# Optimization experiments

Measured on AMD Instinct MI355X. Metric: run time of the kernel, lower is better.

## Reference

```python
import jax, jax.numpy as jnp
import numpy as np
import math

BS, D = 32, 2048  # batch, in_features == out_features (required by the original matmul shapes)
P = 0.5           # DropConnect keep-threshold: mask = (rand <= p)


def setup_inputs() -> dict:
    key = jax.random.key(0)
    kx, kw, kb, kuw, kub = jax.random.split(key, 5)
    stdv = 1.0 / math.sqrt(D)
    x = jax.random.normal(kx, (BS, D), dtype=jnp.float32)
    weight = jax.random.uniform(kw, (D, D), minval=-stdv, maxval=stdv, dtype=jnp.float32)  # (out, in)
    bias = jax.random.uniform(kb, (D,), minval=-stdv, maxval=stdv, dtype=jnp.float32)
    u_w = jax.random.uniform(kuw, (BS, D, D), dtype=jnp.float32)  # per-sample uniforms for weight mask
    u_b = jax.random.uniform(kub, (BS, D), dtype=jnp.float32)     # per-sample uniforms for bias mask
    return {"x": x, "weight": weight, "bias": bias, "u_w": u_w, "u_b": u_b}


def reference(x, weight, bias, u_w, u_b):
    # Training path of DropConnect:
    #   masked_weight[b] = (u_w[b] <= p) * weight            (bs, out, in)
    #   masked_bias[b]   = (u_b[b] <= p) * bias              (bs, out)
    #   y[b] = x[b] @ masked_weight[b] + masked_bias[b]
    # torch.matmul((bs,1,in),(bs,out,in)) contracts x over the 'out' row axis,
    # i.e. y = einsum('bk,bkn->bn') with masked_weight axes (k=out, n=in), valid since out==in.
    wm = (u_w <= P).astype(x.dtype)  # (bs, D, D)
    bm = (u_b <= P).astype(x.dtype)  # (bs, D)
    y = jnp.einsum('bk,bkn->bn', x, wm * weight[None, :, :]) + bm * bias[None, :]
    return y
```

## Files before the change

kernel.cpp:

```cpp
#include <hip/hip_runtime.h>

constexpr int BS = 32;
constexpr int D  = 2048;
constexpr float P = 0.5f;

constexpr int TPB = 256;
constexpr int NPT = 4;
constexpr int NB  = D / (TPB*NPT);
constexpr int KC  = 32;
constexpr int KCH = D / KC;

__global__ __launch_bounds__(TPB) void dropconnect_kernel(
    const float* __restrict__ x,
    const float* __restrict__ weight,
    const float* __restrict__ bias,
    const float* __restrict__ u_w,
    const float* __restrict__ u_b,
    float* __restrict__ out)
{
    const int kc  = blockIdx.x;
    const int nb  = blockIdx.y;
    const int b   = blockIdx.z;
    const int tid = threadIdx.x;

    const int n0 = nb * (TPB * NPT) + tid * NPT;
    const int k0 = kc * KCH;

    __shared__ float xs[KCH];
    if (tid < KCH) xs[tid] = x[b * D + k0 + tid];
    __syncthreads();

    const float4* uw4 = reinterpret_cast<const float4*>(u_w);
    const float4* w4  = reinterpret_cast<const float4*>(weight);
    const int DV = D / 4;

    float acc0 = 0.f, acc1 = 0.f, acc2 = 0.f, acc3 = 0.f;

    size_t iu = ((size_t)b * D + (size_t)k0) * DV + (n0 >> 2);
    size_t iw = (size_t)k0 * DV + (n0 >> 2);

#pragma unroll 4
    for (int kk = 0; kk < KCH; ++kk) {
        const float xv = xs[kk];
        const float4 u = uw4[iu];
        const float4 w = w4[iw];
        acc0 += (u.x <= P) ? xv * w.x : 0.f;
        acc1 += (u.y <= P) ? xv * w.y : 0.f;
        acc2 += (u.z <= P) ? xv * w.z : 0.f;
        acc3 += (u.w <= P) ? xv * w.w : 0.f;
        iu += DV;
        iw += DV;
    }

    if (kc == 0) {
        const float4 ub = reinterpret_cast<const float4*>(u_b)[(b * D + n0) >> 2];
        const float4 bv = reinterpret_cast<const float4*>(bias)[n0 >> 2];
        acc0 += (ub.x <= P) ? bv.x : 0.f;
        acc1 += (ub.y <= P) ? bv.y : 0.f;
        acc2 += (ub.z <= P) ? bv.z : 0.f;
        acc3 += (ub.w <= P) ? bv.w : 0.f;
    }

    float* o = out + (size_t)b * D + n0;
    atomicAdd(o + 0, acc0);
    atomicAdd(o + 1, acc1);
    atomicAdd(o + 2, acc2);
    atomicAdd(o + 3, acc3);
}

extern "C" void kernel_launch(void* const* d_in, const int* in_sizes, int n_in,
                              void* d_out, int out_size, void* d_ws, size_t ws_size,
                              hipStream_t stream) {
    const float* x      = (const float*)d_in[0];
    const float* weight = (const float*)d_in[1];
    const float* bias   = (const float*)d_in[2];
    const float* u_w    = (const float*)d_in[3];
    const float* u_b    = (const float*)d_in[4];
    float* out = (float*)d_out;

    hipMemsetAsync(out, 0, (size_t)out_size * sizeof(float), stream);

    dim3 grid(KC, NB, BS);
    dropconnect_kernel<<<grid, TPB, 0, stream>>>(x, weight, bias, u_w, u_b, out);
}
```

Baseline: 116.4 us.

## Process four batch samples per block to reuse weight loads

Each block now handles four batch samples, loading each weight vector once and applying it against four per-sample mask streams, and the K dimension is split into twice as many chunks. This is meant to cut redundant weight reads and put more independent loads in flight per thread. In exchange it raises register pressure. The kernel stays bound by streaming the large uniform-mask tensor, so the gain may be limited.

New measurement: 152.9 us. 31.3% more time.

```diff
diff --git a/kernel.cpp b/kernel.cpp
--- a/kernel.cpp
+++ b/kernel.cpp
@@ -1,14 +1,19 @@
 #include <hip/hip_runtime.h>
 
-constexpr int BS = 32;
-constexpr int D  = 2048;
+constexpr int BS  = 32;
+constexpr int D   = 2048;
 constexpr float P = 0.5f;
 
 constexpr int TPB = 256;
 constexpr int NPT = 4;
 constexpr int NB  = D / (TPB*NPT);
-constexpr int KC  = 32;
+constexpr int KC  = 64;
 constexpr int KCH = D / KC;
+constexpr int BPB = 4;
+constexpr int BG  = BS / BPB;
+constexpr int DV  = D / 4;
+
+typedef float floatx4 __attribute__((ext_vector_type(4)));
 
 __global__ __launch_bounds__(TPB) void dropconnect_kernel(
     const float* __restrict__ x,
@@ -20,52 +25,67 @@
 {
     const int kc  = blockIdx.x;
     const int nb  = blockIdx.y;
-    const int b   = blockIdx.z;
+    const int bg  = blockIdx.z;
     const int tid = threadIdx.x;
 
     const int n0 = nb * (TPB * NPT) + tid * NPT;
     const int k0 = kc * KCH;
+    const int b0 = bg * BPB;
 
-    __shared__ float xs[KCH];
-    if (tid < KCH) xs[tid] = x[b * D + k0 + tid];
+    __shared__ float xs[BPB][KCH];
+    if (tid < BPB * KCH) {
+        const int bb = tid / KCH, kk = tid % KCH;
+        xs[bb][kk] = x[(b0 + bb) * D + k0 + kk];
+    }
     __syncthreads();
 
-    const float4* uw4 = reinterpret_cast<const float4*>(u_w);
-    const float4* w4  = reinterpret_cast<const float4*>(weight);
-    const int DV = D / 4;
+    const floatx4* uw4 = reinterpret_cast<const floatx4*>(u_w);
+    const floatx4* w4  = reinterpret_cast<const floatx4*>(weight);
 
-    float acc0 = 0.f, acc1 = 0.f, acc2 = 0.f, acc3 = 0.f;
+    float acc[BPB][4] = {};
 
-    size_t iu = ((size_t)b * D + (size_t)k0) * DV + (n0 >> 2);
     size_t iw = (size_t)k0 * DV + (n0 >> 2);
+    size_t iu[BPB];
+#pragma unroll
+    for (int bb = 0; bb < BPB; ++bb)
+        iu[bb] = ((size_t)(b0 + bb) * D + (size_t)k0) * DV + (n0 >> 2);
 
-#pragma unroll 4
+#pragma unroll 2
     for (int kk = 0; kk < KCH; ++kk) {
-        const float xv = xs[kk];
-        const float4 u = uw4[iu];
-        const float4 w = w4[iw];
-        acc0 += (u.x <= P) ? xv * w.x : 0.f;
-        acc1 += (u.y <= P) ? xv * w.y : 0.f;
-        acc2 += (u.z <= P) ? xv * w.z : 0.f;
-        acc3 += (u.w <= P) ? xv * w.w : 0.f;
-        iu += DV;
+        const floatx4 w = w4[iw];
         iw += DV;
+#pragma unroll
+        for (int bb = 0; bb < BPB; ++bb) {
+            const floatx4 u = uw4[iu[bb]];
+            iu[bb] += DV;
+            const float xv = xs[bb][kk];
+            acc[bb][0] += (u.x <= P) ? xv * w.x : 0.f;
+            acc[bb][1] += (u.y <= P) ? xv * w.y : 0.f;
+            acc[bb][2] += (u.z <= P) ? xv * w.z : 0.f;
+            acc[bb][3] += (u.w <= P) ? xv * w.w : 0.f;
+        }
     }
 
     if (kc == 0) {
-        const float4 ub = reinterpret_cast<const float4*>(u_b)[(b * D + n0) >> 2];
-        const float4 bv = reinterpret_cast<const float4*>(bias)[n0 >> 2];
-        acc0 += (ub.x <= P) ? bv.x : 0.f;
-        acc1 += (ub.y <= P) ? bv.y : 0.f;
-        acc2 += (ub.z <= P) ? bv.z : 0.f;
-        acc3 += (ub.w <= P) ? bv.w : 0.f;
+#pragma unroll
+        for (int bb = 0; bb < BPB; ++bb) {
+            const floatx4 ub = reinterpret_cast<const floatx4*>(u_b)[((b0 + bb) * D + n0) >> 2];
+            const floatx4 bv = reinterpret_cast<const floatx4*>(bias)[n0 >> 2];
+            acc[bb][0] += (ub.x <= P) ? bv.x : 0.f;
+            acc[bb][1] += (ub.y <= P) ? bv.y : 0.f;
+            acc[bb][2] += (ub.z <= P) ? bv.z : 0.f;
+            acc[bb][3] += (ub.w <= P) ? bv.w : 0.f;
+        }
     }
 
-    float* o = out + (size_t)b * D + n0;
-    atomicAdd(o + 0, acc0);
-    atomicAdd(o + 1, acc1);
-    atomicAdd(o + 2, acc2);
-    atomicAdd(o + 3, acc3);
+#pragma unroll
+    for (int bb = 0; bb < BPB; ++bb) {
+        float* o = out + (size_t)(b0 + bb) * D + n0;
+        atomicAdd(o + 0, acc[bb][0]);
+        atomicAdd(o + 1, acc[bb][1]);
+        atomicAdd(o + 2, acc[bb][2]);
+        atomicAdd(o + 3, acc[bb][3]);
+    }
 }
 
 extern "C" void kernel_launch(void* const* d_in, const int* in_sizes, int n_in,
@@ -78,8 +98,8 @@
     const float* u_b    = (const float*)d_in[4];
     float* out = (float*)d_out;
 
-    hipMemsetAsync(out, 0, (size_t)out_size * sizeof(float), stream);
+    (void)hipMemsetAsync(out, 0, (size_t)out_size * sizeof(float), stream);
 
-    dim3 grid(KC, NB, BS);
+    dim3 grid(KC, NB, BG);
     dropconnect_kernel<<<grid, TPB, 0, stream>>>(x, weight, bias, u_w, u_b, out);
 }
```
